# Performance work log

Hardware: AMD Instinct MI355X
Metric: run time of the kernel (lower is better)

## Reference

```python
import jax, jax.numpy as jnp
import numpy as np

T, B, IN, H, OUT = 345, 128, 13, 128, 9

# snnTorch ATan surrogate spike: forward = heaviside(x), backward = 1/(1+(pi*x)^2) (alpha=2)
@jax.custom_vjp
def spike_fn(x):
    return (x > 0).astype(x.dtype)

def _spike_fwd(x):
    return spike_fn(x), x

def _spike_bwd(x, g):
    return (g / (1.0 + (jnp.pi * x) ** 2),)

spike_fn.defvjp(_spike_fwd, _spike_bwd)


def setup_inputs() -> dict:
    key = jax.random.key(0)
    ks = jax.random.split(key, 5)
    x = jax.random.normal(ks[0], (B, IN, T), dtype=jnp.float32)
    # PyTorch Linear init: U(-1/sqrt(fan_in), 1/sqrt(fan_in))
    lim1 = 1.0 / np.sqrt(IN)
    lim2 = 1.0 / np.sqrt(H)
    W1 = jax.random.uniform(ks[1], (H, IN), minval=-lim1, maxval=lim1, dtype=jnp.float32)
    b1 = jax.random.uniform(ks[2], (H,), minval=-lim1, maxval=lim1, dtype=jnp.float32)
    W2 = jax.random.uniform(ks[3], (OUT, H), minval=-lim2, maxval=lim2, dtype=jnp.float32)
    b2 = jax.random.uniform(ks[4], (OUT,), minval=-lim2, maxval=lim2, dtype=jnp.float32)
    beta1 = jnp.float32(0.9)
    thr1 = jnp.float32(1.0)
    beta2 = jnp.float32(0.9)
    thr2 = jnp.float32(1.0)
    return {"x": x, "W1": W1, "b1": b1, "W2": W2, "b2": b2,
            "beta1": beta1, "thr1": thr1, "beta2": beta2, "thr2": thr2}


def reference(x, W1, b1, W2, b2, beta1, thr1, beta2, thr2):
    # Precompute fc1 for all steps: (T, B, H)
    cur1_all = jnp.einsum('bct,hc->tbh', x, W1) + b1
    bt1 = jnp.clip(beta1, 0.0, 1.0)
    bt2 = jnp.clip(beta2, 0.0, 1.0)

    def step(carry, cur1):
        mem1, mem2 = carry
        mem1 = bt1 * mem1 + cur1                 # leaky integrate
        spk1 = spike_fn(mem1 - thr1)             # fire
        mem1 = mem1 - spk1 * thr1                # subtract reset
        cur2 = spk1 @ W2.T + b2                  # (B, OUT)
        mem2 = bt2 * mem2 + cur2
        spk2 = spike_fn(mem2 - thr2)
        mem2 = mem2 - spk2 * thr2
        return (mem1, mem2), (spk2, mem2)

    init = (jnp.zeros((B, H), x.dtype), jnp.zeros((B, OUT), x.dtype))
    _, (spk_rec, mem_rec) = jax.lax.scan(step, init, cur1_all)
    return spk_rec, mem_rec  # each (T, B, OUT)
```

## Files before the change

### kernel.cpp

```cpp
#include <hip/hip_runtime.h>

#define T_STEPS 345
#define B_SZ    128
#define IN_SZ   13
#define H_SZ    128
#define OUT_SZ  9
#define XT      348
#define CPAD    388
#define NBO     (B_SZ * OUT_SZ)
#define CHUNK   92
#define BUFR    104


__device__ __forceinline__ void emit_rows(float* __restrict__ buf,
                                          const float* __restrict__ xs,
                                          const float (&w1r)[IN_SZ], float b1r,
                                          int T0, int L, int h, int off, int stride)
{
    int tl = off;
    for (; tl + stride < L; tl += 2 * stride) {
        const int ta = T0 + tl, tb = T0 + tl + stride;
        float ca = b1r, cb = b1r;
#pragma unroll
        for (int c = 0; c < IN_SZ; ++c) {
            ca = fmaf(xs[c * XT + ta], w1r[c], ca);
            cb = fmaf(xs[c * XT + tb], w1r[c], cb);
        }
        buf[tl * H_SZ + h] = ca;
        buf[(tl + stride) * H_SZ + h] = cb;
    }
    if (tl < L) {
        const int ta = T0 + tl;
        float ca = b1r;
#pragma unroll
        for (int c = 0; c < IN_SZ; ++c) ca = fmaf(xs[c * XT + ta], w1r[c], ca);
        buf[tl * H_SZ + h] = ca;
    }
}

__device__ __forceinline__ void scan1_step(float& mem1, float u, float bt1, float th1,
                                           unsigned long long* __restrict__ msh,
                                           int t, bool sl, int half)
{
    mem1 = fmaf(bt1, mem1, u);
    const bool p = mem1 > th1;
    const unsigned long long m = __ballot(p);
    const float ms = mem1 - th1;
    mem1 = p ? ms : mem1;
    if (sl) msh[t * 2 + half] = m;
}

__device__ __forceinline__ void scan1_chunk(const float* __restrict__ buf,
                                            unsigned long long* __restrict__ msh,
                                            int T0, int L, int h,
                                            float bt1, float th1, float& mem1)
{
    const float* cb = buf + h;
    const bool sl = (h & 63) == 0;
    const int half = h >> 6;
    float a0 = cb[0*128], a1 = cb[1*128], a2 = cb[ 2*128], a3 = cb[ 3*128];
    float b0 = cb[4*128], b1v= cb[5*128], b2v= cb[ 6*128], b3 = cb[ 7*128];
    float c0 = cb[8*128], c1v= cb[9*128], c2v= cb[10*128], c3 = cb[11*128];
    const int fullg = L >> 2;
    const int rem   = L & 3;
    for (int g = 0; g < fullg; ++g) {
        const float u0 = a0, u1 = a1, u2 = a2, u3 = a3;
        a0 = b0; a1 = b1v; a2 = b2v; a3 = b3;
        b0 = c0; b1v = c1v; b2v = c2v; b3 = c3;
        const float* nb = cb + (g + 3) * 4 * 128;
        c0 = nb[0]; c1v = nb[128]; c2v = nb[256]; c3 = nb[384];
        const int tb = T0 + g * 4;
        scan1_step(mem1, u0, bt1, th1, msh, tb + 0, sl, half);
        scan1_step(mem1, u1, bt1, th1, msh, tb + 1, sl, half);
        scan1_step(mem1, u2, bt1, th1, msh, tb + 2, sl, half);
        scan1_step(mem1, u3, bt1, th1, msh, tb + 3, sl, half);
    }
    const int tb = T0 + fullg * 4;
    if (rem > 0) scan1_step(mem1, a0, bt1, th1, msh, tb + 0, sl, half);
    if (rem > 1) scan1_step(mem1, a1, bt1, th1, msh, tb + 1, sl, half);
    if (rem > 2) scan1_step(mem1, a2, bt1, th1, msh, tb + 2, sl, half);
}

__device__ __forceinline__ void cur2_task(int j, int tb, int obase, int lane,
                                          const unsigned long long* __restrict__ msh,
                                          const float* __restrict__ W2,
                                          const float* __restrict__ b2,
                                          float* __restrict__ c2s)
{
    const int o_l = j >> 1;
    const int o_u = __builtin_amdgcn_readfirstlane(obase + o_l);
    const int t   = tb + ((j & 1) << 6) + lane;
    const int tc  = (t < T_STEPS) ? t : (T_STEPS - 1);
    const uint4 mm = *(const uint4*)((const char*)msh + (size_t)tc * 16);
    const float* __restrict__ w2row = W2 + o_u * H_SZ;
    float acc = 0.0f;
#pragma unroll
    for (int h = 0; h < 32; ++h)
        acc = fmaf((float)((mm.x >> h) & 1u), w2row[h], acc);
#pragma unroll
    for (int h = 0; h < 32; ++h)
        acc = fmaf((float)((mm.y >> h) & 1u), w2row[32 + h], acc);
#pragma unroll
    for (int h = 0; h < 32; ++h)
        acc = fmaf((float)((mm.z >> h) & 1u), w2row[64 + h], acc);
#pragma unroll
    for (int h = 0; h < 32; ++h)
        acc = fmaf((float)((mm.w >> h) & 1u), w2row[96 + h], acc);
    c2s[(o_u - obase) * CPAD + t] = acc + b2[o_u];
}

template<bool TAIL>
__device__ __forceinline__ void scan2_chunk(const float4* __restrict__ src4, int ci,
                                            float bt2, float th2, float& mem2,
                                            float* __restrict__ out_spk,
                                            float* __restrict__ out_mem)
{
    const int sb = ci * 32;
    float4 fA = src4[sb], fB = src4[sb + 1];
#pragma unroll
    for (int i = 0; i < 32; ++i) {
        const float4 u = fA; fA = fB; fB = src4[sb + i + 2];
        const float vv[4] = { u.x, u.y, u.z, u.w };
#pragma unroll
        for (int kk = 0; kk < 4; ++kk) {
            const int tt = ci * 128 + i * 4 + kk;
            if (!TAIL || tt < T_STEPS) {
                mem2 = fmaf(bt2, mem2, vv[kk]);
                const bool p = mem2 > th2;
                const float s2 = p ? 1.0f : 0.0f;
                const float ms = mem2 - th2;
                mem2 = p ? ms : mem2;
                out_spk[(size_t)tt * NBO] = s2;
                out_mem[(size_t)tt * NBO] = mem2;
            }
        }
    }
}

__global__ __launch_bounds__(1024, 1)
void snn_fused(const float* __restrict__ x, const float* __restrict__ W1,
               const float* __restrict__ b1, const float* __restrict__ W2,
               const float* __restrict__ b2,
               const float* __restrict__ beta1p, const float* __restrict__ thr1p,
               const float* __restrict__ beta2p, const float* __restrict__ thr2p,
               float* __restrict__ out)
{
    const int b    = blockIdx.x >> 1;
    const int half = blockIdx.x & 1;
    const int tid  = threadIdx.x;
    const int wid  = tid >> 6;
    const int lane = tid & 63;
    const int hown = tid & 127;
    const int jsl  = tid >> 7;

    __shared__ __align__(16) float xst[IN_SZ * XT];
    __shared__ __align__(16) float cur1s[2][BUFR * H_SZ];
    __shared__ __align__(16) unsigned long long msh[352 * 2];
    __shared__ __align__(16) float c2s[OUT_SZ * CPAD];

    const float bt1 = fminf(fmaxf(beta1p[0], 0.0f), 1.0f);
    const float th1 = thr1p[0];
    const float bt2 = fminf(fmaxf(beta2p[0], 0.0f), 1.0f);
    const float th2 = thr2p[0];

    const float* xb = x + (size_t)b * (IN_SZ * T_STEPS);
    for (int i = tid; i < IN_SZ * T_STEPS; i += 1024) {
        const int c = i / T_STEPS;
        const int t = i - c * T_STEPS;
        xst[c * XT + t] = xb[i];
    }
    float* W1t = c2s;
    for (int i = tid; i < IN_SZ * H_SZ; i += 1024) {
        const int h = i / IN_SZ;
        const int c = i - IN_SZ * h;
        W1t[c * H_SZ + h] = W1[i];
    }
    __syncthreads();

    float w1r[IN_SZ];
#pragma unroll
    for (int c = 0; c < IN_SZ; ++c) w1r[c] = W1t[c * H_SZ + hown];
    const float b1r = b1[hown];

    const int obase  = half ? 5 : 0;
    const int ntasks = half ? 4 : 5;
    const int NT2    = ntasks * 2;

    emit_rows(cur1s[0], xst, w1r, b1r, 0, CHUNK, hown, jsl, 8);
    __syncthreads();

    float mem1 = 0.0f;
    for (int k = 0; k < 4; ++k) {
        if (tid < 128) {
            const int L = (k < 3) ? CHUNK : (T_STEPS - 3 * CHUNK);
            scan1_chunk(cur1s[k & 1], msh, k * CHUNK, L, tid, bt1, th1, mem1);
        } else if (k < 3) {
            const int kn = k + 1;
            const int L = (kn < 3) ? CHUNK : (T_STEPS - 3 * CHUNK);
            emit_rows(cur1s[kn & 1], xst, w1r, b1r, kn * CHUNK, L, hown, jsl - 1, 7);
        } else {
            const int j = wid - 2;
            if (j < NT2) cur2_task(j, 0, obase, lane, msh, W2, b2, c2s);
        }
        __syncthreads();
    }

    float mem2 = 0.0f;
    const int o_sc = obase + lane;
    float* out_spk = out + (size_t)b * OUT_SZ + o_sc;
    float* out_mem = out_spk + (size_t)T_STEPS * NBO;
    const float4* src4 = (const float4*)(c2s + lane * CPAD);

    if (wid < 15) {
        if (wid < NT2) cur2_task(wid, 128, obase, lane, msh, W2, b2, c2s);
    } else if (lane < ntasks) {
        scan2_chunk<false>(src4, 0, bt2, th2, mem2, out_spk, out_mem);
    }
    __syncthreads();

    if (wid < 15) {
        if (wid < NT2) cur2_task(wid, 256, obase, lane, msh, W2, b2, c2s);
    } else if (lane < ntasks) {
        scan2_chunk<false>(src4, 1, bt2, th2, mem2, out_spk, out_mem);
    }
    __syncthreads();

    if (wid == 15 && lane < ntasks) {
        scan2_chunk<true>(src4, 2, bt2, th2, mem2, out_spk, out_mem);
    }
}

extern "C" void kernel_launch(void* const* d_in, const int* in_sizes, int n_in,
                              void* d_out, int out_size, void* d_ws, size_t ws_size,
                              hipStream_t stream) {
    const float* x     = (const float*)d_in[0];
    const float* W1    = (const float*)d_in[1];
    const float* b1    = (const float*)d_in[2];
    const float* W2    = (const float*)d_in[3];
    const float* b2    = (const float*)d_in[4];
    const float* beta1 = (const float*)d_in[5];
    const float* thr1  = (const float*)d_in[6];
    const float* beta2 = (const float*)d_in[7];
    const float* thr2  = (const float*)d_in[8];
    float* out = (float*)d_out;
    (void)in_sizes; (void)n_in; (void)out_size; (void)d_ws; (void)ws_size;

    snn_fused<<<dim3(B_SZ * 2), dim3(1024), 0, stream>>>(
        x, W1, b1, W2, b2, beta1, thr1, beta2, thr2, out);
}
```

Before: 108.2 us.

## Overlap layer-2 current and scan with layer-1 scan using finer time stripes

Restructures the cross-stage schedule so the fc2 projection and the second-layer scan start while the first-layer scan is still running. Work is cut into 64-step stripes instead of 128-step chunks, and spare waves are spread across emit, cur2 and scan2 roles in each phase. The aim is to shorten the serial tail after the layer-1 scan, at the cost of more complex barrier phasing and fewer waves left for emitting cur1.

```diff
diff --git a/kernel.cpp b/kernel.cpp
--- a/kernel.cpp
+++ b/kernel.cpp
@@ -81,18 +81,16 @@
     if (rem > 2) scan1_step(mem1, a2, bt1, th1, msh, tb + 2, sl, half);
 }
 
-__device__ __forceinline__ void cur2_task(int j, int tb, int obase, int lane,
-                                          const unsigned long long* __restrict__ msh,
-                                          const float* __restrict__ W2,
-                                          const float* __restrict__ b2,
-                                          float* __restrict__ c2s)
-{
-    const int o_l = j >> 1;
-    const int o_u = __builtin_amdgcn_readfirstlane(obase + o_l);
-    const int t   = tb + ((j & 1) << 6) + lane;
-    const int tc  = (t < T_STEPS) ? t : (T_STEPS - 1);
+__device__ __forceinline__ void cur2_otask(int o, int s, int obase, int lane,
+                                           const unsigned long long* __restrict__ msh,
+                                           const float* __restrict__ W2,
+                                           const float* __restrict__ b2,
+                                           float* __restrict__ c2s)
+{
+    const int t  = s * 64 + lane;
+    const int tc = (t < T_STEPS) ? t : (T_STEPS - 1);
     const uint4 mm = *(const uint4*)((const char*)msh + (size_t)tc * 16);
-    const float* __restrict__ w2row = W2 + o_u * H_SZ;
+    const float* __restrict__ w2row = W2 + o * H_SZ;
     float acc = 0.0f;
 #pragma unroll
     for (int h = 0; h < 32; ++h)
@@ -106,24 +104,24 @@
 #pragma unroll
     for (int h = 0; h < 32; ++h)
         acc = fmaf((float)((mm.w >> h) & 1u), w2row[96 + h], acc);
-    c2s[(o_u - obase) * CPAD + t] = acc + b2[o_u];
+    c2s[(o - obase) * CPAD + t] = acc + b2[o];
 }
 
 template<bool TAIL>
-__device__ __forceinline__ void scan2_chunk(const float4* __restrict__ src4, int ci,
-                                            float bt2, float th2, float& mem2,
-                                            float* __restrict__ out_spk,
-                                            float* __restrict__ out_mem)
-{
-    const int sb = ci * 32;
+__device__ __forceinline__ void scan2_stripe(const float4* __restrict__ src4, int s,
+                                             float bt2, float th2, float& mem2,
+                                             float* __restrict__ out_spk,
+                                             float* __restrict__ out_mem)
+{
+    const int sb = s * 16;
     float4 fA = src4[sb], fB = src4[sb + 1];
 #pragma unroll
-    for (int i = 0; i < 32; ++i) {
+    for (int i = 0; i < 16; ++i) {
         const float4 u = fA; fA = fB; fB = src4[sb + i + 2];
         const float vv[4] = { u.x, u.y, u.z, u.w };
 #pragma unroll
         for (int kk = 0; kk < 4; ++kk) {
-            const int tt = ci * 128 + i * 4 + kk;
+            const int tt = s * 64 + i * 4 + kk;
             if (!TAIL || tt < T_STEPS) {
                 mem2 = fmaf(bt2, mem2, vv[kk]);
                 const bool p = mem2 > th2;
@@ -184,49 +182,63 @@
 
     const int obase  = half ? 5 : 0;
     const int ntasks = half ? 4 : 5;
-    const int NT2    = ntasks * 2;
-
-    emit_rows(cur1s[0], xst, w1r, b1r, 0, CHUNK, hown, jsl, 8);
-    __syncthreads();
+    const int L3     = T_STEPS - 3 * CHUNK;
 
     float mem1 = 0.0f;
-    for (int k = 0; k < 4; ++k) {
-        if (tid < 128) {
-            const int L = (k < 3) ? CHUNK : (T_STEPS - 3 * CHUNK);
-            scan1_chunk(cur1s[k & 1], msh, k * CHUNK, L, tid, bt1, th1, mem1);
-        } else if (k < 3) {
-            const int kn = k + 1;
-            const int L = (kn < 3) ? CHUNK : (T_STEPS - 3 * CHUNK);
-            emit_rows(cur1s[kn & 1], xst, w1r, b1r, kn * CHUNK, L, hown, jsl - 1, 7);
-        } else {
-            const int j = wid - 2;
-            if (j < NT2) cur2_task(j, 0, obase, lane, msh, W2, b2, c2s);
-        }
-        __syncthreads();
-    }
-
     float mem2 = 0.0f;
     const int o_sc = obase + lane;
     float* out_spk = out + (size_t)b * OUT_SZ + o_sc;
     float* out_mem = out_spk + (size_t)T_STEPS * NBO;
     const float4* src4 = (const float4*)(c2s + lane * CPAD);
 
-    if (wid < 15) {
-        if (wid < NT2) cur2_task(wid, 128, obase, lane, msh, W2, b2, c2s);
+    emit_rows(cur1s[0], xst, w1r, b1r, 0, CHUNK, hown, jsl, 8);
+    __syncthreads();
+
+    if (tid < 128)      scan1_chunk(cur1s[0], msh, 0, CHUNK, tid, bt1, th1, mem1);
+    else                emit_rows(cur1s[1], xst, w1r, b1r, CHUNK, CHUNK, hown, jsl - 1, 7);
+    __syncthreads();
+
+    if (tid < 128)      scan1_chunk(cur1s[1], msh, CHUNK, CHUNK, tid, bt1, th1, mem1);
+    else if (wid < 14)  emit_rows(cur1s[0], xst, w1r, b1r, 2 * CHUNK, CHUNK, hown, jsl - 1, 6);
+    else {
+        for (int j = wid - 14; j < ntasks; j += 2)
+            cur2_otask(obase + j, 0, obase, lane, msh, W2, b2, c2s);
+    }
+    __syncthreads();
+
+    if (tid < 128)      scan1_chunk(cur1s[0], msh, 2 * CHUNK, CHUNK, tid, bt1, th1, mem1);
+    else if (wid < 14)  emit_rows(cur1s[1], xst, w1r, b1r, 3 * CHUNK, L3, hown, jsl - 1, 6);
+    else if (wid == 14) {
+        for (int j = 0; j < ntasks; ++j)
+            cur2_otask(obase + j, 1, obase, lane, msh, W2, b2, c2s);
     } else if (lane < ntasks) {
-        scan2_chunk<false>(src4, 0, bt2, th2, mem2, out_spk, out_mem);
-    }
-    __syncthreads();
-
-    if (wid < 15) {
-        if (wid < NT2) cur2_task(wid, 256, obase, lane, msh, W2, b2, c2s);
-    } else if (lane < ntasks) {
-        scan2_chunk<false>(src4, 1, bt2, th2, mem2, out_spk, out_mem);
+        scan2_stripe<false>(src4, 0, bt2, th2, mem2, out_spk, out_mem);
+    }
+    __syncthreads();
+
+    if (tid < 128)      scan1_chunk(cur1s[1], msh, 3 * CHUNK, L3, tid, bt1, th1, mem1);
+    else if (wid < 14) {
+        const int idx = wid - 2;
+        if (idx < 2 * ntasks)
+            cur2_otask(obase + idx % ntasks, 2 + idx / ntasks, obase, lane, msh, W2, b2, c2s);
+    } else if (wid == 15 && lane < ntasks) {
+        scan2_stripe<false>(src4, 1, bt2, th2, mem2, out_spk, out_mem);
+    }
+    __syncthreads();
+
+    if (wid >= 2 && wid < 14) {
+        const int idx = wid - 2;
+        if (idx < 2 * ntasks)
+            cur2_otask(obase + idx % ntasks, 4 + idx / ntasks, obase, lane, msh, W2, b2, c2s);
+    } else if (wid == 15 && lane < ntasks) {
+        scan2_stripe<false>(src4, 2, bt2, th2, mem2, out_spk, out_mem);
+        scan2_stripe<false>(src4, 3, bt2, th2, mem2, out_spk, out_mem);
     }
     __syncthreads();
 
     if (wid == 15 && lane < ntasks) {
-        scan2_chunk<true>(src4, 2, bt2, th2, mem2, out_spk, out_mem);
+        scan2_stripe<false>(src4, 4, bt2, th2, mem2, out_spk, out_mem);
+        scan2_stripe<true >(src4, 5, bt2, th2, mem2, out_spk, out_mem);
     }
 }
 
```

After: 117.0 us. 8.2% more time.

## Rebalance cur2/scan2 pipeline into 64-step stripes to shorten serial scan tail

Applied to the files above, without the earlier changes.

Splits the fc2 current computation and the output-layer scan into 64-timestep stripes instead of 128-step chunks. More stripes are computed during the final layer-1 phase, and the remaining stripes are interleaved with scan2 so the single scan wavefront starts earlier and the tail after the last barrier is shorter. The cost is one extra barrier and uneven per-slot work, since scan2 handles two stripes per slot.

```diff
diff --git a/kernel.cpp b/kernel.cpp
--- a/kernel.cpp
+++ b/kernel.cpp
@@ -81,18 +81,16 @@
     if (rem > 2) scan1_step(mem1, a2, bt1, th1, msh, tb + 2, sl, half);
 }
 
-__device__ __forceinline__ void cur2_task(int j, int tb, int obase, int lane,
-                                          const unsigned long long* __restrict__ msh,
-                                          const float* __restrict__ W2,
-                                          const float* __restrict__ b2,
-                                          float* __restrict__ c2s)
-{
-    const int o_l = j >> 1;
-    const int o_u = __builtin_amdgcn_readfirstlane(obase + o_l);
-    const int t   = tb + ((j & 1) << 6) + lane;
-    const int tc  = (t < T_STEPS) ? t : (T_STEPS - 1);
+__device__ __forceinline__ void cur2_stripe(int o, int s, int obase, int lane,
+                                            const unsigned long long* __restrict__ msh,
+                                            const float* __restrict__ W2,
+                                            const float* __restrict__ b2,
+                                            float* __restrict__ c2s)
+{
+    const int t  = s * 64 + lane;
+    const int tc = (t < T_STEPS) ? t : (T_STEPS - 1);
     const uint4 mm = *(const uint4*)((const char*)msh + (size_t)tc * 16);
-    const float* __restrict__ w2row = W2 + o_u * H_SZ;
+    const float* __restrict__ w2row = W2 + o * H_SZ;
     float acc = 0.0f;
 #pragma unroll
     for (int h = 0; h < 32; ++h)
@@ -106,24 +104,24 @@
 #pragma unroll
     for (int h = 0; h < 32; ++h)
         acc = fmaf((float)((mm.w >> h) & 1u), w2row[96 + h], acc);
-    c2s[(o_u - obase) * CPAD + t] = acc + b2[o_u];
+    c2s[(o - obase) * CPAD + t] = acc + b2[o];
 }
 
 template<bool TAIL>
-__device__ __forceinline__ void scan2_chunk(const float4* __restrict__ src4, int ci,
-                                            float bt2, float th2, float& mem2,
-                                            float* __restrict__ out_spk,
-                                            float* __restrict__ out_mem)
-{
-    const int sb = ci * 32;
+__device__ __forceinline__ void scan2_stripe(const float4* __restrict__ src4, int s,
+                                             float bt2, float th2, float& mem2,
+                                             float* __restrict__ out_spk,
+                                             float* __restrict__ out_mem)
+{
+    const int sb = s * 16;
     float4 fA = src4[sb], fB = src4[sb + 1];
 #pragma unroll
-    for (int i = 0; i < 32; ++i) {
+    for (int i = 0; i < 16; ++i) {
         const float4 u = fA; fA = fB; fB = src4[sb + i + 2];
         const float vv[4] = { u.x, u.y, u.z, u.w };
 #pragma unroll
         for (int kk = 0; kk < 4; ++kk) {
-            const int tt = ci * 128 + i * 4 + kk;
+            const int tt = s * 64 + i * 4 + kk;
             if (!TAIL || tt < T_STEPS) {
                 mem2 = fmaf(bt2, mem2, vv[kk]);
                 const bool p = mem2 > th2;
@@ -184,7 +182,6 @@
 
     const int obase  = half ? 5 : 0;
     const int ntasks = half ? 4 : 5;
-    const int NT2    = ntasks * 2;
 
     emit_rows(cur1s[0], xst, w1r, b1r, 0, CHUNK, hown, jsl, 8);
     __syncthreads();
@@ -199,8 +196,8 @@
             const int L = (kn < 3) ? CHUNK : (T_STEPS - 3 * CHUNK);
             emit_rows(cur1s[kn & 1], xst, w1r, b1r, kn * CHUNK, L, hown, jsl - 1, 7);
         } else {
-            const int j = wid - 2;
-            if (j < NT2) cur2_task(j, 0, obase, lane, msh, W2, b2, c2s);
+            for (int idx = wid - 2; idx < 3 * ntasks; idx += 14)
+                cur2_stripe(obase + idx % ntasks, idx / ntasks, obase, lane, msh, W2, b2, c2s);
         }
         __syncthreads();
     }
@@ -211,22 +208,22 @@
     float* out_mem = out_spk + (size_t)T_STEPS * NBO;
     const float4* src4 = (const float4*)(c2s + lane * CPAD);
 
-    if (wid < 15) {
-        if (wid < NT2) cur2_task(wid, 128, obase, lane, msh, W2, b2, c2s);
-    } else if (lane < ntasks) {
-        scan2_chunk<false>(src4, 0, bt2, th2, mem2, out_spk, out_mem);
-    }
-    __syncthreads();
-
-    if (wid < 15) {
-        if (wid < NT2) cur2_task(wid, 256, obase, lane, msh, W2, b2, c2s);
-    } else if (lane < ntasks) {
-        scan2_chunk<false>(src4, 1, bt2, th2, mem2, out_spk, out_mem);
-    }
-    __syncthreads();
+    for (int slot = 0; slot < 3; ++slot) {
+        if (wid >= 2 && wid < 2 + ntasks) {
+            cur2_stripe(obase + (wid - 2), 3 + slot, obase, lane, msh, W2, b2, c2s);
+        } else if (wid == 15 && lane < ntasks) {
+            if (slot == 0) {
+                scan2_stripe<false>(src4, 0, bt2, th2, mem2, out_spk, out_mem);
+            } else {
+                scan2_stripe<false>(src4, 2 * slot - 1, bt2, th2, mem2, out_spk, out_mem);
+                scan2_stripe<false>(src4, 2 * slot,     bt2, th2, mem2, out_spk, out_mem);
+            }
+        }
+        __syncthreads();
+    }
 
     if (wid == 15 && lane < ntasks) {
-        scan2_chunk<true>(src4, 2, bt2, th2, mem2, out_spk, out_mem);
+        scan2_stripe<true>(src4, 5, bt2, th2, mem2, out_spk, out_mem);
     }
 }
 
```

After: 169.4 us. 56.6% more time.
